# Optimization experiments

Measured on AMD Instinct MI355X. Metric: run time of the kernel, lower is better.

The kernel has to match this reference:

```python
import jax, jax.numpy as jnp
import numpy as np
import math

B, C, H, W = 4, 64, 64, 64
N_HEAD = 1
GROUPS = 16
EPS = 1e-5


def dwconv_block(x, w, b, pad):
    # ReflectionPad2d(pad) -> depthwise Conv2d -> LeakyReLU(0.01)
    xp = jnp.pad(x, ((0, 0), (0, 0), (pad, pad), (pad, pad)), mode='reflect')
    y = jax.lax.conv_general_dilated(
        xp, w, window_strides=(1, 1), padding='VALID',
        dimension_numbers=('NCHW', 'OIHW', 'NCHW'),
        feature_group_count=x.shape[1])
    y = y + b[None, :, None, None]
    return jax.nn.leaky_relu(y, 0.01)


def group_norm(x, w, b):
    bb, c, h, ww = x.shape
    xg = x.reshape(bb, GROUPS, c // GROUPS, h, ww)
    mu = xg.mean(axis=(2, 3, 4), keepdims=True)
    var = xg.var(axis=(2, 3, 4), keepdims=True)
    xg = (xg - mu) * jax.lax.rsqrt(var + EPS)
    return xg.reshape(bb, c, h, ww) * w[None, :, None, None] + b[None, :, None, None]


def attention(q, k, v):
    # q,k,v: [B, n_head, head_dim, H, W]; softmax over flattened key grid
    bb, n, d, h, ww = q.shape
    qf = q.reshape(bb, n, d, h * ww)
    kf = k.reshape(bb, n, d, h * ww)
    vf = v.reshape(bb, n, d, h * ww)
    scores = jnp.einsum('bndq,bndk->bnqk', qf, kf) / math.sqrt(C)
    attn = jax.nn.softmax(scores, axis=-1)  # [B,n,HW,HW]
    out = jnp.einsum('bnqk,bndk->bndq', attn, vf)
    return out.reshape(bb, n * d, h, ww)


def conv1x1(x, w, b=None):
    y = jnp.einsum('oc,bchw->bohw', w, x)
    if b is not None:
        y = y + b[None, :, None, None]
    return y


def setup_inputs() -> dict:
    key = jax.random.key(0)
    ks = jax.random.split(key, 16)
    s = lambda fan: 1.0 / math.sqrt(fan)
    return {
        'inputs': jax.random.normal(ks[0], (B, C, H, W), jnp.float32),
        'dw1_w': jax.random.normal(ks[1], (C, 1, 3, 3), jnp.float32) * s(9),
        'dw1_b': jnp.zeros((C,), jnp.float32),
        'dw2_w': jax.random.normal(ks[2], (C, 1, 5, 5), jnp.float32) * s(25),
        'dw2_b': jnp.zeros((C,), jnp.float32),
        'gnA_w': jnp.ones((C,), jnp.float32),
        'gnA_b': jnp.zeros((C,), jnp.float32),
        'gnB_w': jnp.ones((C,), jnp.float32),
        'gnB_b': jnp.zeros((C,), jnp.float32),
        'qkvA_w': jax.random.normal(ks[3], (3 * C, C), jnp.float32) * s(C),
        'qkvB_w': jax.random.normal(ks[4], (3 * C, C), jnp.float32) * s(C),
        'outA_w': jax.random.normal(ks[5], (C, C), jnp.float32) * s(C),
        'outA_b': jnp.zeros((C,), jnp.float32),
        'outB_w': jax.random.normal(ks[6], (C, C), jnp.float32) * s(C),
        'outB_b': jnp.zeros((C,), jnp.float32),
    }


def reference(inputs, dw1_w, dw1_b, dw2_w, dw2_b, gnA_w, gnA_b, gnB_w, gnB_b,
              qkvA_w, qkvB_w, outA_w, outA_b, outB_w, outB_b):
    x = dwconv_block(inputs, dw1_w, dw1_b, pad=1)
    y = dwconv_block(inputs, dw2_w, dw2_b, pad=2)
    head_dim = C // N_HEAD

    x_A = group_norm(x, gnA_w, gnA_b)
    qkv_A = conv1x1(x_A, qkvA_w).reshape(B, N_HEAD, head_dim * 3, H, W)
    qA, kA, vA = jnp.split(qkv_A, 3, axis=2)

    x_B = group_norm(y, gnB_w, gnB_b)
    qkv_B = conv1x1(x_B, qkvB_w).reshape(B, N_HEAD, head_dim * 3, H, W)
    qB, kB, vB = jnp.split(qkv_B, 3, axis=2)

    # branch A: queries from B, keys/values from A
    out_A = conv1x1(attention(qB, kA, vA), outA_w, outA_b) + x_A
    # branch B: queries from A, keys/values from B
    out_B = conv1x1(attention(qA, kB, vB), outB_w, outB_b) + x_B
    return jnp.concatenate((out_A, out_B), axis=1)
```

## Files before the change

### kernel.cpp

```cpp
#include <hip/hip_runtime.h>
#include <hip/hip_bf16.h>

#define HW 4096
#define CCH 64

typedef __attribute__((ext_vector_type(8))) short short8;
typedef __attribute__((ext_vector_type(4))) float f32x4;
typedef unsigned short ushort_t;
typedef unsigned long long u64;

__device__ __forceinline__ unsigned short f2b(float f) {
  unsigned u = __float_as_uint(f);
  return (unsigned short)((u + 0x7fff + ((u >> 16) & 1)) >> 16);
}
__device__ __forceinline__ float b2f(ushort_t u) {
  return __uint_as_float(((unsigned)u) << 16);
}
__device__ __forceinline__ unsigned cvtpk(float lo, float hi) {
  unsigned r;
  asm volatile("v_cvt_pk_bf16_f32 %0, %1, %2" : "=v"(r) : "v"(lo), "v"(hi));
  return r;
}
__device__ __forceinline__ void gload16(const void* g, void* l) {
  __builtin_amdgcn_global_load_lds(
      (const __attribute__((address_space(1))) unsigned int*)g,
      (__attribute__((address_space(3))) unsigned int*)l, 16, 0, 0);
}

__global__ void __launch_bounds__(256) k_dwconv(
    const float* __restrict__ in, const float* __restrict__ w1, const float* __restrict__ b1,
    const float* __restrict__ w2, const float* __restrict__ b2,
    ushort_t* __restrict__ x, ushort_t* __restrict__ y) {
  __shared__ float sm[20 * 68];
  const int bc = blockIdx.x >> 2;
  const int r0 = (blockIdx.x & 3) * 16;
  const int c = bc & 63;
  const float* p = in + bc * HW;
  const int tid = threadIdx.x;
  for (int idx = tid; idx < 20 * 68; idx += 256) {
    int r = r0 + idx / 68 - 2, cc = idx % 68 - 2;
    r = r < 0 ? -r : (r > 63 ? 126 - r : r);
    cc = cc < 0 ? -cc : (cc > 63 ? 126 - cc : cc);
    sm[idx] = p[r * 64 + cc];
  }
  float w1r[9], w2r[25];
  for (int i = 0; i < 9; i++) w1r[i] = w1[c * 9 + i];
  for (int i = 0; i < 25; i++) w2r[i] = w2[c * 25 + i];
  const float bb1 = b1[c], bb2 = b2[c];
  __syncthreads();
  for (int k = 0; k < 4; k++) {
    int pix = tid + k * 256;
    int i = pix >> 6, j = pix & 63;
    float a1 = bb1, a2 = bb2;
    for (int u = 0; u < 3; u++)
      for (int v = 0; v < 3; v++)
        a1 += w1r[u * 3 + v] * sm[(i + 1 + u) * 68 + (j + 1 + v)];
    for (int u = 0; u < 5; u++)
      for (int v = 0; v < 5; v++)
        a2 += w2r[u * 5 + v] * sm[(i + u) * 68 + (j + v)];
    a1 = a1 > 0.f ? a1 : 0.01f * a1;
    a2 = a2 > 0.f ? a2 : 0.01f * a2;
    x[bc * HW + (r0 + i) * 64 + j] = f2b(a1);
    y[bc * HW + (r0 + i) * 64 + j] = f2b(a2);
  }
}

__global__ void __launch_bounds__(256) k_stat(
    const ushort_t* __restrict__ xbf, const ushort_t* __restrict__ ybf,
    const float* __restrict__ gwA, const float* __restrict__ gbA,
    const float* __restrict__ gwB, const float* __restrict__ gbB,
    float* __restrict__ scale, float* __restrict__ shift) {
  const int id = blockIdx.x;
  const int t = id >> 6, b = (id >> 4) & 3, g = id & 15;
  const ushort_t* src = (t ? ybf : xbf) + (b * CCH + g * 4) * HW;
  const int tid = threadIdx.x;
  float s = 0.f, ss = 0.f;
  for (int k = 0; k < 8; k++) {
    const short8 v = *(const short8*)(src + (tid + k * 256) * 8);
    for (int j = 0; j < 8; j++) {
      float f = b2f((ushort_t)v[j]);
      s += f; ss += f * f;
    }
  }
  for (int off = 1; off < 64; off <<= 1) {
    s += __shfl_xor(s, off);
    ss += __shfl_xor(ss, off);
  }
  __shared__ float rs[4], rss[4];
  if ((tid & 63) == 0) { rs[tid >> 6] = s; rss[tid >> 6] = ss; }
  __syncthreads();
  if (tid < 4) {
    s = rs[0] + rs[1] + rs[2] + rs[3];
    ss = rss[0] + rss[1] + rss[2] + rss[3];
    const float mu = s * (1.f / 16384.f);
    const float var = ss * (1.f / 16384.f) - mu * mu;
    const float rsig = rsqrtf(var + 1e-5f);
    const int ch = g * 4 + tid;
    const float gwv = (t ? gwB : gwA)[ch];
    const float a = rsig * gwv;
    scale[t * 256 + b * 64 + ch] = a;
    shift[t * 256 + b * 64 + ch] = (t ? gbB : gbA)[ch] - mu * a;
  }
}

__global__ void __launch_bounds__(256) k_qkv(
    const ushort_t* __restrict__ xbf, const ushort_t* __restrict__ ybf,
    const float* __restrict__ scale, const float* __restrict__ shift,
    const float* __restrict__ wA, const float* __restrict__ wB,
    ushort_t* __restrict__ Qt, ushort_t* __restrict__ Kt, ushort_t* __restrict__ Vv) {
  const int id = blockIdx.x * 256 + threadIdx.x;
  const int pg = id & 1023;
  const int chunk = (id >> 10) % 24;
  const int h = id / (1024 * 24);
  const int b = h >> 1, br = h & 1;
  const ushort_t* X = (br ? ybf : xbf) + b * (CCH * HW);
  const float* W = br ? wB : wA;
  const int sidx = br * 256 + b * 64;
  const int pix0 = pg * 4;
  const int r0 = chunk * 8;
  float acc[8][4];
  for (int r = 0; r < 8; r++) for (int p = 0; p < 4; p++) acc[r][p] = 0.f;
  for (int cc = 0; cc < 64; cc++) {
    const float sc = scale[sidx + cc], sh = shift[sidx + cc];
    const u64 raw = *(const u64*)(X + cc * HW + pix0);
    f32x4 xv;
    for (int p = 0; p < 4; p++)
      xv[p] = b2f((ushort_t)(raw >> (16 * p))) * sc + sh;
    for (int r = 0; r < 8; r++) {
      float wv = W[(r0 + r) * 64 + cc];
      for (int p = 0; p < 4; p++) acc[r][p] += wv * xv[p];
    }
  }
  if (chunk < 16) {
    ushort_t* dst = chunk < 8 ? Qt : Kt;
    const int d0 = (chunk & 7) * 8;
    for (int p = 0; p < 4; p++) {
      short8 v;
      for (int r = 0; r < 8; r++) v[r] = (short)f2b(acc[r][p]);
      *(short8*)(dst + ((h * HW + pix0 + p) << 6) + d0) = v;
    }
  } else {
    const int d0 = (chunk - 16) * 8;
    for (int r = 0; r < 8; r++) {
      ushort_t tmp[4];
      for (int p = 0; p < 4; p++) tmp[p] = f2b(acc[r][p]);
      *(u64*)(Vv + (h * CCH + d0 + r) * HW + pix0) = *(const u64*)tmp;
    }
  }
}

__global__ void __launch_bounds__(512, 2) k_attn(
    const ushort_t* __restrict__ Qt, const ushort_t* __restrict__ Kt,
    const ushort_t* __restrict__ Vv,
    const float* __restrict__ oAw, const float* __restrict__ oAb,
    const float* __restrict__ oBw, const float* __restrict__ oBb,
    const ushort_t* __restrict__ xbf, const ushort_t* __restrict__ ybf,
    const float* __restrict__ scale, const float* __restrict__ shift,
    float* __restrict__ out) {
  __shared__ __align__(16) char lds[49152];
  const int h = blockIdx.x >> 5;
  const int qt = blockIdx.x & 31;
  const int b = h >> 1, br = h & 1;
  const int qh = b * 2 + (1 - br);
  const int tid = threadIdx.x;
  const int lane = tid & 63;
  const int wave = tid >> 6;
  const int q = lane & 15, g = lane >> 4;
  const int qbase = qt * 128 + wave * 16;

  const ushort_t* Qp = Qt + ((qh * HW + qbase + q) << 6);
  const short8 qf0 = *(const short8*)(Qp + g * 8);
  const short8 qf1 = *(const short8*)(Qp + 32 + g * 8);

  const ushort_t* Kh = Kt + ((u64)h * HW << 6);
  const ushort_t* Vh = Vv + (u64)h * (CCH * HW);
  const int rr = tid >> 3;
  const int cc8 = (((tid & 7) ^ (rr & 7)) << 3);
  const ushort_t* gk0 = Kh + (rr << 6) + cc8;
  const ushort_t* gv0 = Vh + rr * HW + cc8;
  char* lK = lds + tid * 16;
  char* lV = lds + 8192 + tid * 16;

  float m_run = -1e30f, l_run = 0.f;
  f32x4 o[4] = {};
  char* wp = lds + 32768 + wave * 2048 + (q << 7);
  const int sw = (q & 7) << 4;
  const int fsw = ((q & 7) << 4);

  gload16(gk0, lK);
  gload16(gv0 + 0, lV);

#pragma unroll 1
  for (int it = 0; it < 64; ++it) {
    if (it < 63) {
      const int nb = (it + 1) & 1;
      gload16(gk0 + ((it + 1) << 12), lK + nb * 16384);
      gload16(gv0 + (it + 1) * 64, lV + nb * 16384);
      asm volatile("s_waitcnt vmcnt(2)" ::: "memory");
    } else {
      asm volatile("s_waitcnt vmcnt(0)" ::: "memory");
    }
    __builtin_amdgcn_s_barrier();

    const char* kb = lds + (it & 1) * 16384;
    const char* vb = kb + 8192;
    short8 ka[4][2], va[4][2];
    for (int c = 0; c < 4; c++)
      for (int s = 0; s < 2; s++)
        ka[c][s] = *(const short8*)(kb + (((c * 16 + q) << 7) | (((s * 4 + g) << 4) ^ fsw)));
    for (int cd = 0; cd < 4; cd++)
      for (int s = 0; s < 2; s++)
        va[cd][s] = *(const short8*)(vb + (((cd * 16 + q) << 7) | (((s * 4 + g) << 4) ^ fsw)));

    f32x4 sa[4];
    for (int c = 0; c < 4; c++) {
      f32x4 zz = {0.f, 0.f, 0.f, 0.f};
      zz = __builtin_amdgcn_mfma_f32_16x16x32_bf16(ka[c][0], qf0, zz, 0, 0, 0);
      sa[c] = __builtin_amdgcn_mfma_f32_16x16x32_bf16(ka[c][1], qf1, zz, 0, 0, 0);
    }
    const float sc = 0.125f * 1.44269504f;
    float z[4][4];
    float mloc = -1e30f;
    for (int c = 0; c < 4; c++)
      for (int i = 0; i < 4; i++) {
        z[c][i] = sa[c][i] * sc;
        mloc = fmaxf(mloc, z[c][i]);
      }
    mloc = fmaxf(mloc, __shfl_xor(mloc, 16));
    mloc = fmaxf(mloc, __shfl_xor(mloc, 32));
    if (!__all(mloc <= m_run + 8.f)) {
      const float mnew = fmaxf(m_run, mloc);
      const float alpha = exp2f(m_run - mnew);
      l_run *= alpha;
      for (int cd = 0; cd < 4; cd++)
        for (int i = 0; i < 4; i++) o[cd][i] *= alpha;
      m_run = mnew;
    }
    float psum = 0.f;
    u64 pk[4];
    for (int c = 0; c < 4; c++) {
      float p0 = exp2f(z[c][0] - m_run), p1 = exp2f(z[c][1] - m_run);
      float p2 = exp2f(z[c][2] - m_run), p3 = exp2f(z[c][3] - m_run);
      psum += p0 + p1 + p2 + p3;
      pk[c] = (u64)cvtpk(p0, p1) | ((u64)cvtpk(p2, p3) << 32);
    }
    psum += __shfl_xor(psum, 16);
    psum += __shfl_xor(psum, 32);
    l_run += psum;
    for (int c = 0; c < 4; c++)
      *(u64*)(wp + (((c << 5) | (g << 3)) ^ sw)) = pk[c];
    asm volatile("s_waitcnt lgkmcnt(0)" ::: "memory");
    __builtin_amdgcn_sched_barrier(0);
    const short8 pb0 = *(const short8*)(wp + ((g << 4) ^ sw));
    const short8 pb1 = *(const short8*)(wp + ((64 | (g << 4)) ^ sw));
    for (int cd = 0; cd < 4; cd++) {
      o[cd] = __builtin_amdgcn_mfma_f32_16x16x32_bf16(va[cd][0], pb0, o[cd], 0, 0, 0);
      o[cd] = __builtin_amdgcn_mfma_f32_16x16x32_bf16(va[cd][1], pb1, o[cd], 0, 0, 0);
    }
    __builtin_amdgcn_s_barrier();
  }

  __syncthreads();
  float* smW = (float*)(lds + wave * 4096);
  const float inv = 1.f / l_run;
  for (int cd = 0; cd < 4; cd++) {
    f32x4 v;
    for (int i = 0; i < 4; i++) v[i] = o[cd][i] * inv;
    *(f32x4*)(smW + q * 64 + (((cd * 4 + g) ^ q) << 2)) = v;
  }
  asm volatile("s_waitcnt lgkmcnt(0)" ::: "memory");
  __builtin_amdgcn_sched_barrier(0);

  const float* W    = br ? oBw : oAw;
  const float* bias = br ? oBb : oAb;
  const ushort_t* xR = (br ? ybf : xbf) + b * (CCH * HW);
  const int sidx = br * 256 + b * 64;
  const int q2 = lane & 15, g2 = lane >> 4;
  const float* smR = (float*)(lds + wave * 4096) + q2 * 64;
  const int pix = qt * 128 + wave * 16 + q2;

  float acc[16];
  for (int oi = 0; oi < 16; oi++) acc[oi] = bias[g2 * 16 + oi];
  for (int c4 = 0; c4 < 16; c4++) {
    const f32x4 Lv = *(const f32x4*)(smR + ((c4 ^ q2) << 2));
    for (int oi = 0; oi < 16; oi++) {
      const f32x4 wv = *(const f32x4*)(W + (g2 * 16 + oi) * 64 + c4 * 4);
      acc[oi] += wv[0] * Lv[0] + wv[1] * Lv[1] + wv[2] * Lv[2] + wv[3] * Lv[3];
    }
  }
  for (int oi = 0; oi < 16; oi++) {
    const int ch = g2 * 16 + oi;
    const float xn = b2f(xR[ch * HW + pix]) * scale[sidx + ch] + shift[sidx + ch];
    out[(b * 128 + br * 64 + ch) * HW + pix] = acc[oi] + xn;
  }
}

extern "C" void kernel_launch(void* const* d_in, const int* in_sizes, int n_in,
                              void* d_out, int out_size, void* d_ws, size_t ws_size,
                              hipStream_t stream) {
  const float* in   = (const float*)d_in[0];
  const float* dw1w = (const float*)d_in[1];
  const float* dw1b = (const float*)d_in[2];
  const float* dw2w = (const float*)d_in[3];
  const float* dw2b = (const float*)d_in[4];
  const float* gnAw = (const float*)d_in[5];
  const float* gnAb = (const float*)d_in[6];
  const float* gnBw = (const float*)d_in[7];
  const float* gnBb = (const float*)d_in[8];
  const float* qAw  = (const float*)d_in[9];
  const float* qBw  = (const float*)d_in[10];
  const float* oAw  = (const float*)d_in[11];
  const float* oAb  = (const float*)d_in[12];
  const float* oBw  = (const float*)d_in[13];
  const float* oBb  = (const float*)d_in[14];
  float* out = (float*)d_out;

  char* ws = (char*)d_ws;
  ushort_t* xbf = (ushort_t*)ws;
  ushort_t* ybf = xbf + 1048576;
  ushort_t* Qt  = ybf + 1048576;
  ushort_t* Kt  = Qt + 2097152;
  ushort_t* Vv  = Kt + 2097152;
  float* scale  = (float*)(Vv + 2097152);
  float* shift  = scale + 512;

  k_dwconv<<<1024, 256, 0, stream>>>(in, dw1w, dw1b, dw2w, dw2b, xbf, ybf);
  k_stat<<<128, 256, 0, stream>>>(xbf, ybf, gnAw, gnAb, gnBw, gnBb, scale, shift);
  k_qkv<<<768, 256, 0, stream>>>(xbf, ybf, scale, shift, qAw, qBw, Qt, Kt, Vv);
  k_attn<<<256, 512, 0, stream>>>(Qt, Kt, Vv, oAw, oAb, oBw, oBb,
                                  xbf, ybf, scale, shift, out);
}
```

Baseline: 228.2 us.

## Fuse group-norm stats into dwconv, retile attention to 128-key blocks with MFMA row sums

Group-norm sums are now accumulated in the depthwise conv kernel with atomics, which removes the separate stats kernel. Scale and shift are recomputed per block from those sums. The softmax scale is folded into Q when it is stored. Attention switches to 256-thread blocks with 64 queries each, loads 128 keys per iteration in two phases, and computes the softmax denominator with an MFMA against a ones vector instead of shuffles. The dwconv kernel is also restructured so each thread computes four pixels from register-cached rows, and the extra memset launch and the atomics add a small fixed cost.

```diff
diff --git a/kernel.cpp b/kernel.cpp
--- a/kernel.cpp
+++ b/kernel.cpp
@@ -9,6 +9,8 @@
 typedef unsigned short ushort_t;
 typedef unsigned long long u64;
 
+#define SCALE_Q 0.18033688f
+
 __device__ __forceinline__ unsigned short f2b(float f) {
   unsigned u = __float_as_uint(f);
   return (unsigned short)((u + 0x7fff + ((u >> 16) & 1)) >> 16);
@@ -30,8 +32,9 @@
 __global__ void __launch_bounds__(256) k_dwconv(
     const float* __restrict__ in, const float* __restrict__ w1, const float* __restrict__ b1,
     const float* __restrict__ w2, const float* __restrict__ b2,
-    ushort_t* __restrict__ x, ushort_t* __restrict__ y) {
+    ushort_t* __restrict__ x, ushort_t* __restrict__ y, float* __restrict__ sums) {
   __shared__ float sm[20 * 68];
+  __shared__ float red[4][4];
   const int bc = blockIdx.x >> 2;
   const int r0 = (blockIdx.x & 3) * 16;
   const int c = bc & 63;
@@ -48,80 +51,89 @@
   for (int i = 0; i < 25; i++) w2r[i] = w2[c * 25 + i];
   const float bb1 = b1[c], bb2 = b2[c];
   __syncthreads();
-  for (int k = 0; k < 4; k++) {
-    int pix = tid + k * 256;
-    int i = pix >> 6, j = pix & 63;
-    float a1 = bb1, a2 = bb2;
+
+  const int i = tid >> 4;
+  const int j0 = (tid & 15) * 4;
+  float rv[5][8];
+  for (int u = 0; u < 5; u++) {
+    *(f32x4*)&rv[u][0] = *(const f32x4*)&sm[(i + u) * 68 + j0];
+    *(f32x4*)&rv[u][4] = *(const f32x4*)&sm[(i + u) * 68 + j0 + 4];
+  }
+  float a1[4], a2[4];
+  for (int px = 0; px < 4; px++) {
+    float s2 = bb2;
+    for (int u = 0; u < 5; u++)
+      for (int v = 0; v < 5; v++) s2 += w2r[u * 5 + v] * rv[u][px + v];
+    float s1 = bb1;
     for (int u = 0; u < 3; u++)
-      for (int v = 0; v < 3; v++)
-        a1 += w1r[u * 3 + v] * sm[(i + 1 + u) * 68 + (j + 1 + v)];
-    for (int u = 0; u < 5; u++)
-      for (int v = 0; v < 5; v++)
-        a2 += w2r[u * 5 + v] * sm[(i + u) * 68 + (j + v)];
-    a1 = a1 > 0.f ? a1 : 0.01f * a1;
-    a2 = a2 > 0.f ? a2 : 0.01f * a2;
-    x[bc * HW + (r0 + i) * 64 + j] = f2b(a1);
-    y[bc * HW + (r0 + i) * 64 + j] = f2b(a2);
-  }
-}
-
-__global__ void __launch_bounds__(256) k_stat(
+      for (int v = 0; v < 3; v++) s1 += w1r[u * 3 + v] * rv[u + 1][px + 1 + v];
+    a1[px] = s1 > 0.f ? s1 : 0.01f * s1;
+    a2[px] = s2 > 0.f ? s2 : 0.01f * s2;
+  }
+  ushort_t t1[4], t2[4];
+  for (int px = 0; px < 4; px++) { t1[px] = f2b(a1[px]); t2[px] = f2b(a2[px]); }
+  const int off = bc * HW + (r0 + i) * 64 + j0;
+  *(u64*)(x + off) = *(const u64*)t1;
+  *(u64*)(y + off) = *(const u64*)t2;
+
+  float s1 = 0, q1 = 0, s2 = 0, q2 = 0;
+  for (int px = 0; px < 4; px++) {
+    s1 += a1[px]; q1 += a1[px] * a1[px];
+    s2 += a2[px]; q2 += a2[px] * a2[px];
+  }
+  for (int o = 1; o < 64; o <<= 1) {
+    s1 += __shfl_xor(s1, o); q1 += __shfl_xor(q1, o);
+    s2 += __shfl_xor(s2, o); q2 += __shfl_xor(q2, o);
+  }
+  if ((tid & 63) == 0) {
+    red[tid >> 6][0] = s1; red[tid >> 6][1] = q1;
+    red[tid >> 6][2] = s2; red[tid >> 6][3] = q2;
+  }
+  __syncthreads();
+  if (tid == 0) {
+    float r4[4];
+    for (int k = 0; k < 4; k++)
+      r4[k] = red[0][k] + red[1][k] + red[2][k] + red[3][k];
+    const int b = bc >> 6, g = (bc & 63) >> 2;
+    const int base = b * 32 + g * 2;
+    atomicAdd(&sums[base], r4[0]);       atomicAdd(&sums[base + 1], r4[1]);
+    atomicAdd(&sums[128 + base], r4[2]); atomicAdd(&sums[128 + base + 1], r4[3]);
+  }
+}
+
+__global__ void __launch_bounds__(256) k_qkv(
     const ushort_t* __restrict__ xbf, const ushort_t* __restrict__ ybf,
+    const float* __restrict__ sums,
     const float* __restrict__ gwA, const float* __restrict__ gbA,
     const float* __restrict__ gwB, const float* __restrict__ gbB,
-    float* __restrict__ scale, float* __restrict__ shift) {
-  const int id = blockIdx.x;
-  const int t = id >> 6, b = (id >> 4) & 3, g = id & 15;
-  const ushort_t* src = (t ? ybf : xbf) + (b * CCH + g * 4) * HW;
-  const int tid = threadIdx.x;
-  float s = 0.f, ss = 0.f;
-  for (int k = 0; k < 8; k++) {
-    const short8 v = *(const short8*)(src + (tid + k * 256) * 8);
-    for (int j = 0; j < 8; j++) {
-      float f = b2f((ushort_t)v[j]);
-      s += f; ss += f * f;
-    }
-  }
-  for (int off = 1; off < 64; off <<= 1) {
-    s += __shfl_xor(s, off);
-    ss += __shfl_xor(ss, off);
-  }
-  __shared__ float rs[4], rss[4];
-  if ((tid & 63) == 0) { rs[tid >> 6] = s; rss[tid >> 6] = ss; }
-  __syncthreads();
-  if (tid < 4) {
-    s = rs[0] + rs[1] + rs[2] + rs[3];
-    ss = rss[0] + rss[1] + rss[2] + rss[3];
-    const float mu = s * (1.f / 16384.f);
-    const float var = ss * (1.f / 16384.f) - mu * mu;
-    const float rsig = rsqrtf(var + 1e-5f);
-    const int ch = g * 4 + tid;
-    const float gwv = (t ? gwB : gwA)[ch];
-    const float a = rsig * gwv;
-    scale[t * 256 + b * 64 + ch] = a;
-    shift[t * 256 + b * 64 + ch] = (t ? gbB : gbA)[ch] - mu * a;
-  }
-}
-
-__global__ void __launch_bounds__(256) k_qkv(
-    const ushort_t* __restrict__ xbf, const ushort_t* __restrict__ ybf,
-    const float* __restrict__ scale, const float* __restrict__ shift,
     const float* __restrict__ wA, const float* __restrict__ wB,
     ushort_t* __restrict__ Qt, ushort_t* __restrict__ Kt, ushort_t* __restrict__ Vv) {
+  __shared__ float scs[64], shs[64];
   const int id = blockIdx.x * 256 + threadIdx.x;
   const int pg = id & 1023;
   const int chunk = (id >> 10) % 24;
   const int h = id / (1024 * 24);
   const int b = h >> 1, br = h & 1;
+  if (threadIdx.x < 64) {
+    const int ch = threadIdx.x, g = ch >> 2;
+    const float s = sums[br * 128 + b * 32 + g * 2];
+    const float ss = sums[br * 128 + b * 32 + g * 2 + 1];
+    const float mu = s * (1.f / 16384.f);
+    const float var = ss * (1.f / 16384.f) - mu * mu;
+    const float rsig = rsqrtf(var + 1e-5f);
+    const float a = rsig * (br ? gwB : gwA)[ch];
+    scs[ch] = a;
+    shs[ch] = (br ? gbB : gbA)[ch] - mu * a;
+  }
+  __syncthreads();
   const ushort_t* X = (br ? ybf : xbf) + b * (CCH * HW);
   const float* W = br ? wB : wA;
-  const int sidx = br * 256 + b * 64;
   const int pix0 = pg * 4;
   const int r0 = chunk * 8;
   float acc[8][4];
   for (int r = 0; r < 8; r++) for (int p = 0; p < 4; p++) acc[r][p] = 0.f;
   for (int cc = 0; cc < 64; cc++) {
-    const float sc = scale[sidx + cc], sh = shift[sidx + cc];
+    const float sc = scs[cc], sh = shs[cc];
     const u64 raw = *(const u64*)(X + cc * HW + pix0);
     f32x4 xv;
     for (int p = 0; p < 4; p++)
@@ -133,10 +145,11 @@
   }
   if (chunk < 16) {
     ushort_t* dst = chunk < 8 ? Qt : Kt;
+    const float qs = chunk < 8 ? SCALE_Q : 1.0f;
     const int d0 = (chunk & 7) * 8;
     for (int p = 0; p < 4; p++) {
       short8 v;
-      for (int r = 0; r < 8; r++) v[r] = (short)f2b(acc[r][p]);
+      for (int r = 0; r < 8; r++) v[r] = (short)f2b(acc[r][p] * qs);
       *(short8*)(dst + ((h * HW + pix0 + p) << 6) + d0) = v;
     }
   } else {
@@ -149,24 +162,40 @@
   }
 }
 
-__global__ void __launch_bounds__(512, 2) k_attn(
+__global__ void __launch_bounds__(256, 2) k_attn(
     const ushort_t* __restrict__ Qt, const ushort_t* __restrict__ Kt,
     const ushort_t* __restrict__ Vv,
     const float* __restrict__ oAw, const float* __restrict__ oAb,
     const float* __restrict__ oBw, const float* __restrict__ oBb,
     const ushort_t* __restrict__ xbf, const ushort_t* __restrict__ ybf,
-    const float* __restrict__ scale, const float* __restrict__ shift,
+    const float* __restrict__ sums,
+    const float* __restrict__ gwA, const float* __restrict__ gbA,
+    const float* __restrict__ gwB, const float* __restrict__ gbB,
     float* __restrict__ out) {
-  __shared__ __align__(16) char lds[49152];
-  const int h = blockIdx.x >> 5;
-  const int qt = blockIdx.x & 31;
+  __shared__ __align__(16) char lds[74240];
+  const int h = blockIdx.x >> 6;
+  const int qt = blockIdx.x & 63;
   const int b = h >> 1, br = h & 1;
   const int qh = b * 2 + (1 - br);
   const int tid = threadIdx.x;
   const int lane = tid & 63;
   const int wave = tid >> 6;
   const int q = lane & 15, g = lane >> 4;
-  const int qbase = qt * 128 + wave * 16;
+  const int qbase = qt * 64 + wave * 16;
+
+  float* scs = (float*)(lds + 73728);
+  float* shs = scs + 64;
+  if (tid < 64) {
+    const int ch = tid, gg = ch >> 2;
+    const float s = sums[br * 128 + b * 32 + gg * 2];
+    const float ss = sums[br * 128 + b * 32 + gg * 2 + 1];
+    const float mu = s * (1.f / 16384.f);
+    const float var = ss * (1.f / 16384.f) - mu * mu;
+    const float rsig = rsqrtf(var + 1e-5f);
+    const float a = rsig * (br ? gwB : gwA)[ch];
+    scs[ch] = a;
+    shs[ch] = (br ? gbB : gbA)[ch] - mu * a;
+  }
 
   const ushort_t* Qp = Qt + ((qh * HW + qbase + q) << 6);
   const short8 qf0 = *(const short8*)(Qp + g * 8);
@@ -174,95 +203,101 @@
 
   const ushort_t* Kh = Kt + ((u64)h * HW << 6);
   const ushort_t* Vh = Vv + (u64)h * (CCH * HW);
-  const int rr = tid >> 3;
-  const int cc8 = (((tid & 7) ^ (rr & 7)) << 3);
-  const ushort_t* gk0 = Kh + (rr << 6) + cc8;
-  const ushort_t* gv0 = Vh + rr * HW + cc8;
-  char* lK = lds + tid * 16;
-  char* lV = lds + 8192 + tid * 16;
-
-  float m_run = -1e30f, l_run = 0.f;
+  const ushort_t* gk[4];
+  const ushort_t* gv[4];
+  for (int j = 0; j < 4; j++) {
+    const int idx = j * 256 + tid;
+    const int rK = idx >> 3, cK = (idx & 7) ^ (rK & 7);
+    gk[j] = Kh + (rK << 6) + (cK << 3);
+    const int rV = idx >> 4, cV = (idx & 15) ^ (rV & 7);
+    gv[j] = Vh + rV * HW + (cV << 3);
+  }
+  char* lK = lds + (tid << 4);
+  char* lV = lds + 16384 + (tid << 4);
+
+  float m_run = -1e30f;
   f32x4 o[4] = {};
-  char* wp = lds + 32768 + wave * 2048 + (q << 7);
+  f32x4 accl = {};
+  char* wp = lds + 65536 + wave * 2048 + (q << 7);
   const int sw = (q & 7) << 4;
-  const int fsw = ((q & 7) << 4);
-
-  gload16(gk0, lK);
-  gload16(gv0 + 0, lV);
+  short8 ones;
+  for (int j = 0; j < 8; j++) ones[j] = (short)0x3F80;
+
+  for (int j = 0; j < 4; j++) gload16(gk[j], lK + j * 4096);
+  for (int j = 0; j < 4; j++) gload16(gv[j], lV + j * 4096);
 
 #pragma unroll 1
-  for (int it = 0; it < 64; ++it) {
-    if (it < 63) {
+  for (int it = 0; it < 32; ++it) {
+    if (it < 31) {
       const int nb = (it + 1) & 1;
-      gload16(gk0 + ((it + 1) << 12), lK + nb * 16384);
-      gload16(gv0 + (it + 1) * 64, lV + nb * 16384);
-      asm volatile("s_waitcnt vmcnt(2)" ::: "memory");
+      for (int j = 0; j < 4; j++) gload16(gk[j] + (it + 1) * 8192, lK + nb * 32768 + j * 4096);
+      for (int j = 0; j < 4; j++) gload16(gv[j] + (it + 1) * 128, lV + nb * 32768 + j * 4096);
+      asm volatile("s_waitcnt vmcnt(8)" ::: "memory");
     } else {
       asm volatile("s_waitcnt vmcnt(0)" ::: "memory");
     }
     __builtin_amdgcn_s_barrier();
 
-    const char* kb = lds + (it & 1) * 16384;
-    const char* vb = kb + 8192;
-    short8 ka[4][2], va[4][2];
-    for (int c = 0; c < 4; c++)
-      for (int s = 0; s < 2; s++)
-        ka[c][s] = *(const short8*)(kb + (((c * 16 + q) << 7) | (((s * 4 + g) << 4) ^ fsw)));
-    for (int cd = 0; cd < 4; cd++)
-      for (int s = 0; s < 2; s++)
-        va[cd][s] = *(const short8*)(vb + (((cd * 16 + q) << 7) | (((s * 4 + g) << 4) ^ fsw)));
-
-    f32x4 sa[4];
-    for (int c = 0; c < 4; c++) {
-      f32x4 zz = {0.f, 0.f, 0.f, 0.f};
-      zz = __builtin_amdgcn_mfma_f32_16x16x32_bf16(ka[c][0], qf0, zz, 0, 0, 0);
-      sa[c] = __builtin_amdgcn_mfma_f32_16x16x32_bf16(ka[c][1], qf1, zz, 0, 0, 0);
-    }
-    const float sc = 0.125f * 1.44269504f;
-    float z[4][4];
-    float mloc = -1e30f;
-    for (int c = 0; c < 4; c++)
-      for (int i = 0; i < 4; i++) {
-        z[c][i] = sa[c][i] * sc;
-        mloc = fmaxf(mloc, z[c][i]);
+    const char* kb = lds + (it & 1) * 32768;
+    const char* vb = kb + 16384;
+#pragma unroll
+    for (int ph = 0; ph < 2; ph++) {
+      short8 ka[4][2], va[4][2];
+      for (int c = 0; c < 4; c++)
+        for (int s = 0; s < 2; s++)
+          ka[c][s] = *(const short8*)(kb + ((ph * 64 + c * 16 + q) << 7) +
+                                      (((s * 4 + g) ^ (q & 7)) << 4));
+      for (int cd = 0; cd < 4; cd++)
+        for (int s = 0; s < 2; s++)
+          va[cd][s] = *(const short8*)(vb + ((cd * 16 + q) << 8) +
+                                       (((ph * 8 + s * 4 + g) ^ (q & 7)) << 4));
+
+      f32x4 sa[4];
+      for (int c = 0; c < 4; c++) {
+        f32x4 zz = {0.f, 0.f, 0.f, 0.f};
+        zz = __builtin_amdgcn_mfma_f32_16x16x32_bf16(ka[c][0], qf0, zz, 0, 0, 0);
+        sa[c] = __builtin_amdgcn_mfma_f32_16x16x32_bf16(ka[c][1], qf1, zz, 0, 0, 0);
       }
-    mloc = fmaxf(mloc, __shfl_xor(mloc, 16));
-    mloc = fmaxf(mloc, __shfl_xor(mloc, 32));
-    if (!__all(mloc <= m_run + 8.f)) {
-      const float mnew = fmaxf(m_run, mloc);
-      const float alpha = exp2f(m_run - mnew);
-      l_run *= alpha;
-      for (int cd = 0; cd < 4; cd++)
-        for (int i = 0; i < 4; i++) o[cd][i] *= alpha;
-      m_run = mnew;
-    }
-    float psum = 0.f;
-    u64 pk[4];
-    for (int c = 0; c < 4; c++) {
-      float p0 = exp2f(z[c][0] - m_run), p1 = exp2f(z[c][1] - m_run);
-      float p2 = exp2f(z[c][2] - m_run), p3 = exp2f(z[c][3] - m_run);
-      psum += p0 + p1 + p2 + p3;
-      pk[c] = (u64)cvtpk(p0, p1) | ((u64)cvtpk(p2, p3) << 32);
-    }
-    psum += __shfl_xor(psum, 16);
-    psum += __shfl_xor(psum, 32);
-    l_run += psum;
-    for (int c = 0; c < 4; c++)
-      *(u64*)(wp + (((c << 5) | (g << 3)) ^ sw)) = pk[c];
-    asm volatile("s_waitcnt lgkmcnt(0)" ::: "memory");
-    __builtin_amdgcn_sched_barrier(0);
-    const short8 pb0 = *(const short8*)(wp + ((g << 4) ^ sw));
-    const short8 pb1 = *(const short8*)(wp + ((64 | (g << 4)) ^ sw));
-    for (int cd = 0; cd < 4; cd++) {
-      o[cd] = __builtin_amdgcn_mfma_f32_16x16x32_bf16(va[cd][0], pb0, o[cd], 0, 0, 0);
-      o[cd] = __builtin_amdgcn_mfma_f32_16x16x32_bf16(va[cd][1], pb1, o[cd], 0, 0, 0);
+      float m0 = fmaxf(fmaxf(fmaxf(sa[0][0], sa[0][1]), sa[0][2]), sa[0][3]);
+      float m1 = fmaxf(fmaxf(fmaxf(sa[1][0], sa[1][1]), sa[1][2]), sa[1][3]);
+      float m2 = fmaxf(fmaxf(fmaxf(sa[2][0], sa[2][1]), sa[2][2]), sa[2][3]);
+      float m3 = fmaxf(fmaxf(fmaxf(sa[3][0], sa[3][1]), sa[3][2]), sa[3][3]);
+      float mloc = fmaxf(fmaxf(m0, m1), fmaxf(m2, m3));
+      mloc = fmaxf(mloc, __shfl_xor(mloc, 16));
+      mloc = fmaxf(mloc, __shfl_xor(mloc, 32));
+      if (!__all(mloc <= m_run + 8.f)) {
+        const float mnew = fmaxf(m_run, mloc);
+        const float alpha = exp2f(m_run - mnew);
+        for (int cd = 0; cd < 4; cd++)
+          for (int i = 0; i < 4; i++) o[cd][i] *= alpha;
+        for (int i = 0; i < 4; i++) accl[i] *= alpha;
+        m_run = mnew;
+      }
+      u64 pk[4];
+      for (int c = 0; c < 4; c++) {
+        float p0 = exp2f(sa[c][0] - m_run), p1 = exp2f(sa[c][1] - m_run);
+        float p2 = exp2f(sa[c][2] - m_run), p3 = exp2f(sa[c][3] - m_run);
+        pk[c] = (u64)cvtpk(p0, p1) | ((u64)cvtpk(p2, p3) << 32);
+      }
+      for (int c = 0; c < 4; c++)
+        *(u64*)(wp + (((c << 5) | (g << 3)) ^ sw)) = pk[c];
+      asm volatile("s_waitcnt lgkmcnt(0)" ::: "memory");
+      __builtin_amdgcn_sched_barrier(0);
+      const short8 pb0 = *(const short8*)(wp + ((g << 4) ^ sw));
+      const short8 pb1 = *(const short8*)(wp + ((64 | (g << 4)) ^ sw));
+      for (int cd = 0; cd < 4; cd++) {
+        o[cd] = __builtin_amdgcn_mfma_f32_16x16x32_bf16(va[cd][0], pb0, o[cd], 0, 0, 0);
+        o[cd] = __builtin_amdgcn_mfma_f32_16x16x32_bf16(va[cd][1], pb1, o[cd], 0, 0, 0);
+      }
+      accl = __builtin_amdgcn_mfma_f32_16x16x32_bf16(ones, pb0, accl, 0, 0, 0);
+      accl = __builtin_amdgcn_mfma_f32_16x16x32_bf16(ones, pb1, accl, 0, 0, 0);
     }
     __builtin_amdgcn_s_barrier();
   }
 
   __syncthreads();
   float* smW = (float*)(lds + wave * 4096);
-  const float inv = 1.f / l_run;
+  const float inv = 1.f / accl[0];
   for (int cd = 0; cd < 4; cd++) {
     f32x4 v;
     for (int i = 0; i < 4; i++) v[i] = o[cd][i] * inv;
@@ -274,10 +309,9 @@
   const float* W    = br ? oBw : oAw;
   const float* bias = br ? oBb : oAb;
   const ushort_t* xR = (br ? ybf : xbf) + b * (CCH * HW);
-  const int sidx = br * 256 + b * 64;
   const int q2 = lane & 15, g2 = lane >> 4;
   const float* smR = (float*)(lds + wave * 4096) + q2 * 64;
-  const int pix = qt * 128 + wave * 16 + q2;
+  const int pix = qt * 64 + wave * 16 + q2;
 
   float acc[16];
   for (int oi = 0; oi < 16; oi++) acc[oi] = bias[g2 * 16 + oi];
@@ -290,7 +324,7 @@
   }
   for (int oi = 0; oi < 16; oi++) {
     const int ch = g2 * 16 + oi;
-    const float xn = b2f(xR[ch * HW + pix]) * scale[sidx + ch] + shift[sidx + ch];
+    const float xn = b2f(xR[ch * HW + pix]) * scs[ch] + shs[ch];
     out[(b * 128 + br * 64 + ch) * HW + pix] = acc[oi] + xn;
   }
 }
@@ -321,12 +355,12 @@
   ushort_t* Qt  = ybf + 1048576;
   ushort_t* Kt  = Qt + 2097152;
   ushort_t* Vv  = Kt + 2097152;
-  float* scale  = (float*)(Vv + 2097152);
-  float* shift  = scale + 512;
-
-  k_dwconv<<<1024, 256, 0, stream>>>(in, dw1w, dw1b, dw2w, dw2b, xbf, ybf);
-  k_stat<<<128, 256, 0, stream>>>(xbf, ybf, gnAw, gnAb, gnBw, gnBb, scale, shift);
-  k_qkv<<<768, 256, 0, stream>>>(xbf, ybf, scale, shift, qAw, qBw, Qt, Kt, Vv);
-  k_attn<<<256, 512, 0, stream>>>(Qt, Kt, Vv, oAw, oAb, oBw, oBb,
-                                  xbf, ybf, scale, shift, out);
-}
+  float* sums   = (float*)(Vv + 2097152);
+
+  hipMemsetAsync(sums, 0, 256 * sizeof(float), stream);
+  k_dwconv<<<1024, 256, 0, stream>>>(in, dw1w, dw1b, dw2w, dw2b, xbf, ybf, sums);
+  k_qkv<<<768, 256, 0, stream>>>(xbf, ybf, sums, gnAw, gnAb, gnBw, gnBb,
+                                 qAw, qBw, Qt, Kt, Vv);
+  k_attn<<<512, 256, 0, stream>>>(Qt, Kt, Vv, oAw, oAb, oBw, oBb,
+                                  xbf, ybf, sums, gnAw, gnAb, gnBw, gnBb, out);
+}
```

Result: no change. 224.7 us (-1.5%).
